# Kernel tuning notes

Hardware: AMD Instinct MI355X
Metric: run time of the kernel (lower is better)

## Reference

```python
import jax, jax.numpy as jnp
import numpy as np

B, N, DIM, VDIM, H, HD = 4, 1369, 1024, 1536, 16, 64
ROPE_HW, ROPE_DIM, THETA = 37, 32, 10000.0
LN_EPS = 1e-5


def _rope_tables():
    # VisionRotaryEmbeddingFast: freqs_for='lang', dim=32, pt_seq_len=ft_seq_len=37
    inv = 1.0 / THETA ** (jnp.arange(0, ROPE_DIM, 2, dtype=jnp.float32) / ROPE_DIM)  # [16]
    t = jnp.arange(ROPE_HW, dtype=jnp.float32) / ROPE_HW * ROPE_HW                    # [37]
    f = t[:, None] * inv[None, :]                                                     # [37,16]
    f = jnp.repeat(f, 2, axis=-1)                                                     # [37,32]
    # broadcat along last dim over the 2D grid -> [37,37,64]
    f2 = jnp.concatenate([jnp.broadcast_to(f[:, None, :], (ROPE_HW, ROPE_HW, ROPE_DIM)),
                          jnp.broadcast_to(f[None, :, :], (ROPE_HW, ROPE_HW, ROPE_DIM))], axis=-1)
    f2 = f2.reshape(-1, 2 * ROPE_DIM)                                                 # [1369,64]
    return jnp.cos(f2), jnp.sin(f2)


def _rotate_half(x):
    # pairs (x0,x1) -> (-x1,x0), interleaved
    xr = x.reshape(*x.shape[:-1], x.shape[-1] // 2, 2)
    x1, x2 = xr[..., 0], xr[..., 1]
    return jnp.stack((-x2, x1), axis=-1).reshape(x.shape)


def setup_inputs() -> dict:
    key = jax.random.key(0)
    ks = jax.random.split(key, 8)
    return {
        "x": jax.random.normal(ks[0], (B, N, DIM), jnp.float32),
        "value": jax.random.normal(ks[1], (B, N, VDIM), jnp.float32),
        "attn_mask": jax.random.randint(ks[2], (B, N), 0, 2).astype(bool),
        "wq": jax.random.normal(ks[3], (DIM, DIM), jnp.float32) * 0.02,
        "wk": jax.random.normal(ks[4], (DIM, VDIM), jnp.float32) * 0.02,
        "wv": jax.random.normal(ks[5], (DIM, VDIM), jnp.float32) * 0.02,
        "ln_g": jnp.ones((DIM,), jnp.float32),
        "ln_b": jnp.zeros((DIM,), jnp.float32),
        "wp": jax.random.normal(ks[6], (DIM, DIM), jnp.float32) * 0.02,
        "bp": jnp.zeros((DIM,), jnp.float32),
    }


def reference(x, value, attn_mask, wq, wk, wv, ln_g, ln_b, wp, bp):
    cos, sin = _rope_tables()  # [N, 64] each
    # projections (torch F.linear: y = x @ W.T)
    q = jnp.einsum('bni,oi->bno', x, wq).reshape(B, N, H, HD).transpose(0, 2, 1, 3)
    k = jnp.einsum('bni,oi->bno', value, wk).reshape(B, N, H, HD).transpose(0, 2, 1, 3)
    v = jnp.einsum('bni,oi->bno', value, wv).reshape(B, N, H, HD).transpose(0, 2, 1, 3)
    # inline RoPE on q and k
    q = q * cos + _rotate_half(q) * sin
    k = k * cos + _rotate_half(k) * sin
    q = q * (HD ** -0.5)
    attn = jnp.einsum('bhnd,bhmd->bhnm', q, k)
    neg_inf = jnp.finfo(attn.dtype).min
    attn = jnp.where(attn_mask[:, None, None, :], attn, neg_inf)
    attn = jax.nn.softmax(attn, axis=-1)
    out = jnp.einsum('bhnm,bhmd->bhnd', attn, v)
    out = out.transpose(0, 2, 1, 3).reshape(B, N, H * HD)
    # inner_attn_ln (LayerNorm, eps=1e-5)
    mu = jnp.mean(out, axis=-1, keepdims=True)
    var = jnp.var(out, axis=-1, keepdims=True)
    out = (out - mu) * jax.lax.rsqrt(var + LN_EPS) * ln_g + ln_b
    # output projection
    return jnp.einsum('bni,oi->bno', out, wp) + bp
```

## Files before the change

kernel.cpp:

```cpp
#include <hip/hip_runtime.h>
#include <hip/hip_bf16.h>

#define BB 4
#define NN 1369
#define DIMM 1024
#define VDIMM 1536
#define HH 16
#define MM (BB*NN)
#define MPAD 5504
#define NPAD 1408
#define KVB 64
#define NT (NPAD/KVB)
#define QSCALE 0.18028334f

typedef __attribute__((ext_vector_type(4))) float f32x4;
typedef __attribute__((ext_vector_type(8))) __bf16 bf16x8;
typedef __attribute__((ext_vector_type(4))) __bf16 bf16x4;

#define GLOAD_LDS(gsrc, ldst) \
  __builtin_amdgcn_global_load_lds((const __attribute__((address_space(1))) unsigned int*)(gsrc), \
                                   (__attribute__((address_space(3))) unsigned int*)(ldst), 16, 0, 0)

__global__ __launch_bounds__(256) void cvt4(const float* __restrict__ src,
                                            __bf16* __restrict__ dst, int n4) {
  int i = blockIdx.x * blockDim.x + threadIdx.x;
  int st = gridDim.x * blockDim.x;
  for (; i < n4; i += st) {
    f32x4 v = ((const f32x4*)src)[i];
    bf16x4 o;
    o[0] = (__bf16)v[0]; o[1] = (__bf16)v[1];
    o[2] = (__bf16)v[2]; o[3] = (__bf16)v[3];
    ((bf16x4*)dst)[i] = o;
  }
}

__global__ __launch_bounds__(256) void rope_tables(float* __restrict__ cosT,
                                                   float* __restrict__ sinT) {
  int idx = blockIdx.x * blockDim.x + threadIdx.x;
  if (idx >= NN * 64) return;
  int n = idx >> 6, d = idx & 63;
  int r = n / 37, c = n % 37;
  int m = (d < 32) ? (d >> 1) : ((d - 32) >> 1);
  float p = (d < 32) ? (float)r : (float)c;
  float inv = powf(10000.f, -(float)m * (1.f / 16.f));
  float a = p * inv;
  cosT[idx] = cosf(a);
  sinT[idx] = sinf(a);
}

__global__ __launch_bounds__(256) void mask_prep(const void* __restrict__ mask,
                                                 float* __restrict__ maskA) {
  __shared__ int flags[2];
  int t = threadIdx.x;
  if (t < 2) flags[t] = 0;
  __syncthreads();
  const unsigned int* mw = (const unsigned int*)mask;
  for (int i = t; i < NN; i += blockDim.x) {
    unsigned int w = mw[i];
    if (w == 0x3F800000u) atomicOr(&flags[1], 1);
    else if (w > 1u) atomicOr(&flags[0], 1);
  }
  __syncthreads();
  int md = flags[1] ? 2 : (flags[0] ? 1 : 0);
  const unsigned char* mb = (const unsigned char*)mask;
  const float* mf = (const float*)mask;
  for (int i = t; i < BB * NPAD; i += blockDim.x) {
    int b = i / NPAD, key = i % NPAD;
    float v = -1e30f;
    if (key < NN) {
      int idx = b * NN + key;
      bool on = (md == 0) ? (mw[idx] != 0u) : (md == 1) ? (mb[idx] != 0) : (mf[idx] != 0.f);
      if (on) v = 0.f;
    }
    maskA[i] = v;
  }
}

template <int TN, int EPI>
__global__ __launch_bounds__(256) void gemm_bt(
    const __bf16* __restrict__ A, const __bf16* __restrict__ W, int K,
    __bf16* __restrict__ obf, __bf16* __restrict__ obf2, float* __restrict__ of32,
    const float* __restrict__ cosT, const float* __restrict__ sinT,
    const float* __restrict__ bp) {
  constexpr int MI = (TN == 128) ? 4 : 2;
  __shared__ __bf16 As[2][128 * 32];
  __shared__ __bf16 Bs[2][TN * 32];
  const int tid = threadIdx.x;
  const int w = tid >> 6, l = tid & 63;
  const int i0 = blockIdx.x;
  const int orig = (i0 & 7) * 86 + (i0 >> 3);
  const int tN = orig & 15, tM = orig >> 4;
  const int wm = (TN == 128) ? (w >> 1) : w;
  const int wn = (TN == 128) ? (w & 1) : 0;
  const int wmo = wm * ((TN == 128) ? 64 : 32);
  const int lo = l & 15, hi = l >> 4;

  const __bf16* Asrc = A + (size_t)(tM * 128 + lo) * K + hi * 8;
  const __bf16* Wsrc = W + (size_t)(tN * TN + lo) * K + hi * 8;

  f32x4 zero = {0.f, 0.f, 0.f, 0.f};
  f32x4 acc[MI][4];
#pragma unroll
  for (int i = 0; i < MI; ++i)
#pragma unroll
    for (int j = 0; j < 4; ++j) acc[i][j] = zero;

#define GSTAGE(buf, k0)                                                          \
  {                                                                              \
    _Pragma("unroll") for (int j = 0; j < 2; ++j) {                              \
      const int c = j * 4 + w;                                                   \
      GLOAD_LDS(Asrc + (size_t)c * 16 * K + (k0), (char*)&As[buf][c * 512]);     \
    }                                                                            \
    if (TN == 128) {                                                             \
      _Pragma("unroll") for (int j = 0; j < 2; ++j) {                            \
        const int c = j * 4 + w;                                                 \
        GLOAD_LDS(Wsrc + (size_t)c * 16 * K + (k0), (char*)&Bs[buf][c * 512]);   \
      }                                                                          \
    } else {                                                                     \
      GLOAD_LDS(Wsrc + (size_t)w * 16 * K + (k0), (char*)&Bs[buf][w * 512]);     \
    }                                                                            \
  }

  GSTAGE(0, 0);
  int cur = 0;
  const int nk = K >> 5;
  const int ga = wmo >> 4;
  const int gb = (TN == 128) ? (wn * 4) : 0;
  for (int t = 0; t < nk; ++t) {
    __syncthreads();
    if (t + 1 < nk) GSTAGE(cur ^ 1, (t + 1) * 32);
    bf16x8 af[MI], bfr[4];
#pragma unroll
    for (int mi = 0; mi < MI; ++mi)
      af[mi] = *(const bf16x8*)&As[cur][(ga + mi) * 512 + hi * 128 + lo * 8];
#pragma unroll
    for (int ni = 0; ni < 4; ++ni)
      bfr[ni] = *(const bf16x8*)&Bs[cur][(gb + ni) * 512 + hi * 128 + lo * 8];
#pragma unroll
    for (int mi = 0; mi < MI; ++mi)
#pragma unroll
      for (int ni = 0; ni < 4; ++ni)
        acc[mi][ni] = __builtin_amdgcn_mfma_f32_16x16x32_bf16(af[mi], bfr[ni], acc[mi][ni], 0, 0, 0);
    cur ^= 1;
  }
#undef GSTAGE

  const int m_base = tM * 128 + wmo;
  const int o_base = tN * TN + wn * 64;
  const bool isK = (EPI == 1) && (tN < 8);
#pragma unroll
  for (int mi = 0; mi < MI; ++mi) {
    const int m4 = m_base + mi * 16 + hi * 4;
    if (EPI == 1 && !isK) {
      if (m4 < MM) {
        const int b0 = m4 / NN, n0 = m4 % NN;
#pragma unroll
        for (int ni = 0; ni < 4; ++ni) {
          const int o2 = o_base + ni * 16 + lo - 1024;
          const int h = o2 >> 6, d = o2 & 63;
          if (n0 <= NN - 4) {
            bf16x4 pv;
#pragma unroll
            for (int r = 0; r < 4; ++r) pv[r] = (__bf16)acc[mi][ni][r];
            *(bf16x4*)&obf2[((size_t)(b0 * HH + h) * 64 + d) * NPAD + n0] = pv;
          } else {
#pragma unroll
            for (int r = 0; r < 4; ++r) {
              const int mr = m4 + r;
              const int br = mr / NN, nr = mr % NN;
              obf2[((size_t)(br * HH + h) * 64 + d) * NPAD + nr] = (__bf16)acc[mi][ni][r];
            }
          }
        }
      }
    } else {
#pragma unroll
      for (int r = 0; r < 4; ++r) {
        const int mrow = m4 + r;
#pragma unroll
        for (int ni = 0; ni < 4; ++ni) {
          const int col = o_base + ni * 16 + lo;
          float v = acc[mi][ni][r];
          if (EPI == 0 || EPI == 1) {
            float pprt = __shfl_xor(v, 1);
            if (mrow < MM) {
              int b = mrow / NN, n = mrow % NN;
              int h = col >> 6, d = col & 63;
              float cs = cosT[n * 64 + d], sn = sinT[n * 64 + d];
              float out = v * cs + (((d & 1) == 0) ? -pprt : pprt) * sn;
              if (EPI == 0) out *= QSCALE;
              obf[((size_t)(b * HH + h) * NPAD + n) * 64 + d] = (__bf16)out;
            }
          } else {
            if (mrow < MM) of32[(size_t)mrow * DIMM + col] = v + bp[col];
          }
        }
      }
    }
  }
}

__device__ inline unsigned int pk2(float a, float b) {
  unsigned int ua = (unsigned int)__builtin_bit_cast(unsigned short, (__bf16)a);
  unsigned int ub = (unsigned int)__builtin_bit_cast(unsigned short, (__bf16)b);
  return ua | (ub << 16);
}

__global__ __launch_bounds__(256) void attn_kernel(
    const __bf16* __restrict__ Qb, const __bf16* __restrict__ Kb,
    const __bf16* __restrict__ Vtb, const float* __restrict__ maskA,
    float* __restrict__ AO) {
  __shared__ __bf16 Ks[2][64 * 64];
  __shared__ __bf16 Vs[2][64 * 64];
  __shared__ unsigned int Plds[4][16 * 32];
  const int tid = threadIdx.x;
  const int w = tid >> 6, l = tid & 63;
  const int lo = l & 15, hi = l >> 4;

  const int i = blockIdx.x;
  const int orig = (i & 7) * 176 + (i >> 3);
  const int bh = orig / NT;
  const int qt = orig % NT;
  const int b = bh >> 4;
  const int q0 = qt * 64 + w * 16;

  const __bf16* Qp = Qb + ((size_t)bh * NPAD + q0) * 64;
  bf16x8 qf0 = *(const bf16x8*)&Qp[lo * 64 + hi * 8];
  bf16x8 qf1 = *(const bf16x8*)&Qp[lo * 64 + 32 + hi * 8];

  const int row8 = l >> 3;
  const int swz16 = ((l & 7) ^ row8) << 4;
  const int lo7 = lo & 7;
  const int swzW = (lo & 7) << 2;

  f32x4 zero = {0.f, 0.f, 0.f, 0.f};
  f32x4 O[4];
#pragma unroll
  for (int n = 0; n < 4; ++n) O[n] = zero;
  float lr = 0.f;
  const float* mk = maskA + b * NPAD;

#define STAGE(buf, k0)                                                                   \
  {                                                                                      \
    _Pragma("unroll") for (int j = 0; j < 2; ++j) {                                      \
      const int rbase = (j * 4 + w) * 8;                                                 \
      const char* ksrc = (const char*)Kb +                                               \
          ((size_t)bh * NPAD + (k0) + rbase + row8) * 128 + swz16;                       \
      GLOAD_LDS(ksrc, (char*)&Ks[buf][0] + rbase * 128);                                 \
      const char* vsrc = (const char*)Vtb +                                              \
          ((size_t)(bh * 64 + rbase + row8) * NPAD + (k0)) * 2 + swz16;                  \
      GLOAD_LDS(vsrc, (char*)&Vs[buf][0] + rbase * 128);                                 \
    }                                                                                    \
  }

  STAGE(0, 0);
  __syncthreads();
  int cur = 0;

  for (int t = 0; t < NT; ++t) {
    if (t + 1 < NT) STAGE(cur ^ 1, (t + 1) * KVB);

    const __bf16* KB = &Ks[cur][0];
    const __bf16* VB = &Vs[cur][0];

    f32x4 mv[4];
#pragma unroll
    for (int c = 0; c < 4; ++c) mv[c] = *(const f32x4*)&mk[t * KVB + c * 16 + hi * 4];

    f32x4 S[4];
    __builtin_amdgcn_s_setprio(1);
#pragma unroll
    for (int c = 0; c < 4; ++c) {
      const int kr = c * 16 + lo;
      bf16x8 kfa = *(const bf16x8*)&KB[kr * 64 + ((hi ^ lo7) * 8)];
      bf16x8 kfb = *(const bf16x8*)&KB[kr * 64 + (((hi + 4) ^ lo7) * 8)];
      f32x4 s = __builtin_amdgcn_mfma_f32_16x16x32_bf16(kfa, qf0, zero, 0, 0, 0);
      S[c]     = __builtin_amdgcn_mfma_f32_16x16x32_bf16(kfb, qf1, s, 0, 0, 0);
    }
    __builtin_amdgcn_s_setprio(0);

    float rs = 0.f;
#pragma unroll
    for (int c = 0; c < 4; ++c) {
      float p0 = exp2f(S[c][0] + mv[c][0]);
      float p1 = exp2f(S[c][1] + mv[c][1]);
      float p2 = exp2f(S[c][2] + mv[c][2]);
      float p3 = exp2f(S[c][3] + mv[c][3]);
      rs += (p0 + p1) + (p2 + p3);
      uint2 pw = {pk2(p0, p1), pk2(p2, p3)};
      *(uint2*)&Plds[w][lo * 32 + ((8 * c + 2 * hi) ^ swzW)] = pw;
    }
    lr += rs;

    bf16x8 pf0 = *(const bf16x8*)&Plds[w][lo * 32 + ((4 * hi) ^ swzW)];
    bf16x8 pf1 = *(const bf16x8*)&Plds[w][lo * 32 + ((16 + 4 * hi) ^ swzW)];

    __builtin_amdgcn_s_setprio(1);
#pragma unroll
    for (int n = 0; n < 4; ++n) {
      const int vr = n * 16 + lo;
      bf16x8 vfa = *(const bf16x8*)&VB[vr * 64 + ((hi ^ lo7) * 8)];
      bf16x8 vfb = *(const bf16x8*)&VB[vr * 64 + (((hi + 4) ^ lo7) * 8)];
      O[n] = __builtin_amdgcn_mfma_f32_16x16x32_bf16(vfa, pf0, O[n], 0, 0, 0);
      O[n] = __builtin_amdgcn_mfma_f32_16x16x32_bf16(vfb, pf1, O[n], 0, 0, 0);
    }
    __builtin_amdgcn_s_setprio(0);

    __syncthreads();
    cur ^= 1;
  }
#undef STAGE

  lr += __shfl_xor(lr, 16);
  lr += __shfl_xor(lr, 32);
  const float inv = 1.f / lr;

  const int h = bh & 15;
  const int token = q0 + lo;
  if (token < NN) {
    float* dst = AO + (size_t)(b * NN + token) * DIMM + h * 64 + hi * 4;
#pragma unroll
    for (int n = 0; n < 4; ++n) {
      f32x4 o = O[n];
      o[0] *= inv; o[1] *= inv; o[2] *= inv; o[3] *= inv;
      *(f32x4*)(dst + n * 16) = o;
    }
  }
}

__global__ __launch_bounds__(256) void ln_kernel(
    const float* __restrict__ AO, const float* __restrict__ g,
    const float* __restrict__ be, __bf16* __restrict__ outb) {
  const int row = blockIdx.x;
  const int t = threadIdx.x;
  const float* x = AO + (size_t)row * DIMM;
  f32x4 v = ((const f32x4*)x)[t];
  float s = v[0] + v[1] + v[2] + v[3];
  float sq = v[0] * v[0] + v[1] * v[1] + v[2] * v[2] + v[3] * v[3];
#pragma unroll
  for (int m = 1; m < 64; m <<= 1) { s += __shfl_xor(s, m); sq += __shfl_xor(sq, m); }
  __shared__ float ss[4], ssq[4];
  int w = t >> 6, l = t & 63;
  if (l == 0) { ss[w] = s; ssq[w] = sq; }
  __syncthreads();
  s = ss[0] + ss[1] + ss[2] + ss[3];
  sq = ssq[0] + ssq[1] + ssq[2] + ssq[3];
  float mean = s * (1.f / 1024.f);
  float var = sq * (1.f / 1024.f) - mean * mean;
  float rstd = rsqrtf(var + 1e-5f);
  __bf16* o = outb + (size_t)row * DIMM + t * 4;
  const float* gp = g + t * 4;
  const float* bp2 = be + t * 4;
#pragma unroll
  for (int j = 0; j < 4; ++j) o[j] = (__bf16)((v[j] - mean) * rstd * gp[j] + bp2[j]);
}

extern "C" void kernel_launch(void* const* d_in, const int* in_sizes, int n_in,
                              void* d_out, int out_size, void* d_ws, size_t ws_size,
                              hipStream_t stream) {
  const float* x   = (const float*)d_in[0];
  const float* val = (const float*)d_in[1];
  const void*  msk = d_in[2];
  const float* wq  = (const float*)d_in[3];
  const float* wk  = (const float*)d_in[4];
  const float* wv  = (const float*)d_in[5];
  const float* lng = (const float*)d_in[6];
  const float* lnb = (const float*)d_in[7];
  const float* wp  = (const float*)d_in[8];
  const float* bpv = (const float*)d_in[9];
  float* out = (float*)d_out;

  char* ws = (char*)d_ws;
  size_t off = 0;
  auto alloc = [&](size_t bytes) -> char* {
    char* p = ws + off;
    off += (bytes + 255) & ~(size_t)255;
    return p;
  };
  __bf16* xb   = (__bf16*)alloc((size_t)MPAD * 1024 * 2);
  __bf16* vb   = (__bf16*)alloc((size_t)MPAD * 1536 * 2);
  __bf16* wqb  = (__bf16*)alloc((size_t)1024 * 1024 * 2);
  __bf16* wkvb = (__bf16*)alloc((size_t)2048 * 1536 * 2);
  __bf16* wpb  = (__bf16*)alloc((size_t)1024 * 1024 * 2);
  __bf16* Qb   = (__bf16*)alloc((size_t)64 * NPAD * 64 * 2);
  __bf16* Kb   = (__bf16*)alloc((size_t)64 * NPAD * 64 * 2);
  __bf16* Vtb  = (__bf16*)alloc((size_t)64 * 64 * NPAD * 2);
  float* AO    = (float*)alloc((size_t)MM * 1024 * 4);
  float* cosT  = (float*)alloc((size_t)NN * 64 * 4);
  float* sinT  = (float*)alloc((size_t)NN * 64 * 4);
  float* maskA = (float*)alloc((size_t)BB * NPAD * 4);

  hipMemsetAsync(xb + (size_t)MM * 1024, 0, (size_t)(MPAD - MM) * 1024 * 2, stream);
  hipMemsetAsync(vb + (size_t)MM * 1536, 0, (size_t)(MPAD - MM) * 1536 * 2, stream);
  hipMemsetAsync(Qb, 0, (size_t)64 * NPAD * 64 * 2, stream);
  hipMemsetAsync(Kb, 0, (size_t)64 * NPAD * 64 * 2, stream);
  hipMemsetAsync(Vtb, 0, (size_t)64 * 64 * NPAD * 2, stream);

  cvt4<<<1024, 256, 0, stream>>>(x, xb, MM * 1024 / 4);
  cvt4<<<1024, 256, 0, stream>>>(val, vb, MM * 1536 / 4);
  cvt4<<<512, 256, 0, stream>>>(wq, wqb, 1024 * 1024 / 4);
  cvt4<<<512, 256, 0, stream>>>(wk, wkvb, 1024 * 1536 / 4);
  cvt4<<<512, 256, 0, stream>>>(wv, wkvb + (size_t)1024 * 1536, 1024 * 1536 / 4);
  cvt4<<<512, 256, 0, stream>>>(wp, wpb, 1024 * 1024 / 4);
  rope_tables<<<(NN * 64 + 255) / 256, 256, 0, stream>>>(cosT, sinT);
  mask_prep<<<1, 256, 0, stream>>>(msk, maskA);

  gemm_bt<64, 0><<<dim3(688), 256, 0, stream>>>(xb, wqb, 1024, Qb, nullptr, nullptr, cosT, sinT, nullptr);
  gemm_bt<128, 1><<<dim3(688), 256, 0, stream>>>(vb, wkvb, 1536, Kb, Vtb, nullptr, cosT, sinT, nullptr);

  attn_kernel<<<dim3(64 * NT), 256, 0, stream>>>(Qb, Kb, Vtb, maskA, AO);

  ln_kernel<<<MM, 256, 0, stream>>>(AO, lng, lnb, xb);

  gemm_bt<64, 3><<<dim3(688), 256, 0, stream>>>(xb, wpb, 1024, nullptr, nullptr, out, nullptr, nullptr, bpv);
}
```

Baseline: 305.7 us.

## Triple-buffer GEMM LDS stages with explicit vmcnt waits and MFMA priority

```diff
diff --git a/kernel.cpp b/kernel.cpp
--- a/kernel.cpp
+++ b/kernel.cpp
@@ -83,8 +83,8 @@
     const float* __restrict__ cosT, const float* __restrict__ sinT,
     const float* __restrict__ bp) {
   constexpr int MI = (TN == 128) ? 4 : 2;
-  __shared__ __bf16 As[2][128 * 32];
-  __shared__ __bf16 Bs[2][TN * 32];
+  __shared__ __bf16 As[3][128 * 32];
+  __shared__ __bf16 Bs[3][TN * 32];
   const int tid = threadIdx.x;
   const int w = tid >> 6, l = tid & 63;
   const int i0 = blockIdx.x;
@@ -105,45 +105,53 @@
 #pragma unroll
     for (int j = 0; j < 4; ++j) acc[i][j] = zero;
 
-#define GSTAGE(buf, k0)                                                          \
-  {                                                                              \
-    _Pragma("unroll") for (int j = 0; j < 2; ++j) {                              \
-      const int c = j * 4 + w;                                                   \
-      GLOAD_LDS(Asrc + (size_t)c * 16 * K + (k0), (char*)&As[buf][c * 512]);     \
-    }                                                                            \
-    if (TN == 128) {                                                             \
-      _Pragma("unroll") for (int j = 0; j < 2; ++j) {                            \
-        const int c = j * 4 + w;                                                 \
-        GLOAD_LDS(Wsrc + (size_t)c * 16 * K + (k0), (char*)&Bs[buf][c * 512]);   \
-      }                                                                          \
-    } else {                                                                     \
-      GLOAD_LDS(Wsrc + (size_t)w * 16 * K + (k0), (char*)&Bs[buf][w * 512]);     \
-    }                                                                            \
-  }
-
+  auto GSTAGE = [&](int buf, int k0) {
+#pragma unroll
+    for (int j = 0; j < 2; ++j) {
+      const int c = j * 4 + w;
+      GLOAD_LDS(Asrc + (size_t)c * 16 * K + k0, (char*)&As[buf][c * 512]);
+    }
+    if constexpr (TN == 128) {
+#pragma unroll
+      for (int j = 0; j < 2; ++j) {
+        const int c = j * 4 + w;
+        GLOAD_LDS(Wsrc + (size_t)c * 16 * K + k0, (char*)&Bs[buf][c * 512]);
+      }
+    } else {
+      GLOAD_LDS(Wsrc + (size_t)w * 16 * K + k0, (char*)&Bs[buf][w * 512]);
+    }
+  };
+
+  const int nk = K >> 5;
   GSTAGE(0, 0);
-  int cur = 0;
-  const int nk = K >> 5;
+  GSTAGE(1, 32);
   const int ga = wmo >> 4;
   const int gb = (TN == 128) ? (wn * 4) : 0;
   for (int t = 0; t < nk; ++t) {
-    __syncthreads();
-    if (t + 1 < nk) GSTAGE(cur ^ 1, (t + 1) * 32);
+    if (t < nk - 1) {
+      if constexpr (TN == 128) asm volatile("s_waitcnt vmcnt(4)" ::: "memory");
+      else                     asm volatile("s_waitcnt vmcnt(3)" ::: "memory");
+    } else {
+      asm volatile("s_waitcnt vmcnt(0)" ::: "memory");
+    }
+    asm volatile("s_barrier" ::: "memory");
+    const int cb = t % 3;
     bf16x8 af[MI], bfr[4];
 #pragma unroll
     for (int mi = 0; mi < MI; ++mi)
-      af[mi] = *(const bf16x8*)&As[cur][(ga + mi) * 512 + hi * 128 + lo * 8];
+      af[mi] = *(const bf16x8*)&As[cb][(ga + mi) * 512 + hi * 128 + lo * 8];
 #pragma unroll
     for (int ni = 0; ni < 4; ++ni)
-      bfr[ni] = *(const bf16x8*)&Bs[cur][(gb + ni) * 512 + hi * 128 + lo * 8];
+      bfr[ni] = *(const bf16x8*)&Bs[cb][(gb + ni) * 512 + hi * 128 + lo * 8];
+    if (t + 2 < nk) GSTAGE((t + 2) % 3, (t + 2) * 32);
+    __builtin_amdgcn_s_setprio(1);
 #pragma unroll
     for (int mi = 0; mi < MI; ++mi)
 #pragma unroll
       for (int ni = 0; ni < 4; ++ni)
         acc[mi][ni] = __builtin_amdgcn_mfma_f32_16x16x32_bf16(af[mi], bfr[ni], acc[mi][ni], 0, 0, 0);
-    cur ^= 1;
-  }
-#undef GSTAGE
+    __builtin_amdgcn_s_setprio(0);
+  }
 
   const int m_base = tM * 128 + wmo;
   const int o_base = tN * TN + wn * 64;
```

Result: no change. 306.5 us (+0.3%).
